# Kernel optimization log

Measured on AMD Instinct MI355X. Metric: run time of the kernel, lower is better.

## Reference

```python
import jax, jax.numpy as jnp
import numpy as np

B, D, L = 2, 1024, 4096   # batch, channels (= num_heads), seq len
FS = 4                    # filter_size
DEPTH = 11                # ceil(log2((L-1)/(FS-1)+1))
LN_EPS = 1e-5


def setup_inputs() -> dict:
    key = jax.random.key(0)
    ks = jax.random.split(key, 7)
    return {
        "x": jax.random.normal(ks[0], (B, D, L), jnp.float32),
        "h0": jax.random.normal(ks[1], (D, 1, FS), jnp.float32) * 0.2,
        "h1": jax.random.normal(ks[2], (D, 1, FS), jnp.float32) * 0.2,
        "w_mix": jax.random.normal(ks[3], (D, D), jnp.float32) / np.sqrt(D),
        "b_mix": jnp.zeros((D,), jnp.float32),
        "ln_gamma": jnp.ones((D,), jnp.float32),
        "ln_beta": jnp.zeros((D,), jnp.float32),
    }


def _dw_conv(a, h, dilation):
    # depthwise (groups = D) dilated conv1d, cross-correlation like torch
    return jax.lax.conv_general_dilated(
        a, h, window_strides=(1,), padding='VALID',
        rhs_dilation=(dilation,),
        dimension_numbers=('NCH', 'OIH', 'NCH'),
        feature_group_count=D)


def reference(x, h0, h1, w_mix, b_mix, ln_gamma, ln_beta):
    # --- multires conv tree ---
    a = x
    dilation = 1
    a_list, b_list = [], []
    for _ in range(DEPTH):
        pad = dilation * (FS - 1)
        ap = jnp.pad(a, ((0, 0), (0, 0), (pad, 0)))  # left causal pad
        b = _dw_conv(ap, h1, dilation)
        a = _dw_conv(ap, h0, dilation)
        a_list.append(a)
        b_list.append(b)
        dilation *= 2
    # --- gated combination across scales (deepest level first) ---
    a_rev = a_list[::-1]
    b_rev = b_list[::-1]
    y = jnp.zeros_like(x)
    gated = None
    for i in range(DEPTH):
        if i + 1 < DEPTH:
            gated = jax.nn.sigmoid(a_rev[i]) * b_rev[i + 1]
        # last iteration reuses the previous gated tensor (matches original)
        y = y + gated
    # --- 1x1 channel mix (Dropout1d is identity in eval) + residual ---
    mixed = jnp.einsum('oc,bcl->bol', w_mix, y) + b_mix[None, :, None]
    z = mixed + x
    # --- LayerNorm over channel dim ---
    mu = jnp.mean(z, axis=1, keepdims=True)
    var = jnp.mean(jnp.square(z - mu), axis=1, keepdims=True)
    out = (z - mu) * jax.lax.rsqrt(var + LN_EPS)
    out = out * ln_gamma[None, :, None] + ln_beta[None, :, None]
    return out
```

## Files before the change

kernel.cpp:

```cpp
#include <hip/hip_runtime.h>
#include <hip/hip_bf16.h>

#define NB 2
#define ND 1024
#define NL 4096
#define NFS 4
#define NDEPTH 11
#define LN_EPS 1e-5f

#define BM 128
#define BN 128
#define BK 32
#define NKI (ND / BK)
#define ASZ (BM * BK)

#define CPAD 3072
#define CBUF (CPAD + NL)

typedef __bf16 bf16x8 __attribute__((ext_vector_type(8)));
typedef float f32x4 __attribute__((ext_vector_type(4)));
typedef _Float16 half8 __attribute__((ext_vector_type(8)));

__device__ __forceinline__ unsigned short f2bf(float f) {
    __hip_bfloat16 h = __float2bfloat16(f);
    unsigned short u;
    __builtin_memcpy(&u, &h, 2);
    return u;
}

__device__ __forceinline__ float bf2f(unsigned short u) {
    unsigned int ui = (unsigned int)u << 16;
    float f;
    __builtin_memcpy(&f, &ui, 4);
    return f;
}

__device__ __forceinline__ unsigned int pack2bf(float lo, float hi) {
    return (unsigned int)f2bf(lo) | ((unsigned int)f2bf(hi) << 16);
}

__device__ __forceinline__ float sigm(float v) {
    return __builtin_amdgcn_rcpf(1.f + __expf(-v));
}

__device__ __forceinline__ void llds16(const void* g, void* l) {
    __builtin_amdgcn_global_load_lds(
        (const __attribute__((address_space(1))) unsigned int*)g,
        (__attribute__((address_space(3))) unsigned int*)l, 16, 0, 0);
}

__global__ __launch_bounds__(256) void wconv_kernel(const float* __restrict__ w,
                                                    unsigned short* __restrict__ wbf) {
    const int idx8 = (blockIdx.x * 256 + threadIdx.x) * 8;
    const float4 v0 = *reinterpret_cast<const float4*>(w + idx8);
    const float4 v1 = *reinterpret_cast<const float4*>(w + idx8 + 4);
    uint4 o;
    o.x = pack2bf(v0.x, v0.y);
    o.y = pack2bf(v0.z, v0.w);
    o.z = pack2bf(v1.x, v1.y);
    o.w = pack2bf(v1.z, v1.w);
    *reinterpret_cast<uint4*>(wbf + idx8) = o;
}

__global__ __launch_bounds__(512, 8) void conv_cascade_kernel(const float* __restrict__ x,
                                                              const float* __restrict__ h0,
                                                              const float* __restrict__ h1,
                                                              unsigned short* __restrict__ ybf) {
    __shared__ _Float16 a_sh[CBUF];
    const int row = blockIdx.x;
    const int d = row & (ND - 1);
    const int t = threadIdx.x;

    if (t < CPAD / 8) *reinterpret_cast<half8*>(&a_sh[t * 8]) = (half8)0;

    const float* xrow = x + (size_t)row * NL;

    _Float16 h0c[NFS], h1c[NFS];
#pragma unroll
    for (int k = 0; k < NFS; ++k) {
        h0c[k] = (_Float16)h0[d * NFS + k];
        h1c[k] = (_Float16)h1[d * NFS + k];
    }

    half8 cur;
    {
        const float4 v0 = *reinterpret_cast<const float4*>(xrow + t * 8);
        const float4 v1 = *reinterpret_cast<const float4*>(xrow + t * 8 + 4);
        cur[0] = (_Float16)v0.x; cur[1] = (_Float16)v0.y;
        cur[2] = (_Float16)v0.z; cur[3] = (_Float16)v0.w;
        cur[4] = (_Float16)v1.x; cur[5] = (_Float16)v1.y;
        cur[6] = (_Float16)v1.z; cur[7] = (_Float16)v1.w;
    }
    const int A = CPAD + t * 8;
    *reinterpret_cast<half8*>(&a_sh[A]) = cur;

    float yacc[8];
    half8 bprev = (half8)0;
#pragma unroll
    for (int j = 0; j < 8; ++j) yacc[j] = 0.f;
    __syncthreads();

    half8 an, bn;

#define CONV_MATH(a1, a2, a3)                                       \
    an = cur * h0c[3] + (a1)*h0c[2] + (a2)*h0c[1] + (a3)*h0c[0];    \
    bn = cur * h1c[3] + (a1)*h1c[2] + (a2)*h1c[1] + (a3)*h1c[0];

#define CONV_FIN(SC)                                                \
    {                                                               \
        *reinterpret_cast<half8*>(&a_sh[A]) = an;                   \
        if ((SC) > 0.f) {                                           \
            _Pragma("unroll") for (int j = 0; j < 8; ++j)           \
                yacc[j] += (SC)*sigm((float)an[j]) * (float)bprev[j]; \
        }                                                           \
        cur = an;                                                   \
        bprev = bn;                                                 \
    }

    {
        const half8 m = *reinterpret_cast<const half8*>(&a_sh[A - 8]);
        const half8 a1 = __builtin_shufflevector(m, cur, 7, 8, 9, 10, 11, 12, 13, 14);
        const half8 a2 = __builtin_shufflevector(m, cur, 6, 7, 8, 9, 10, 11, 12, 13);
        const half8 a3 = __builtin_shufflevector(m, cur, 5, 6, 7, 8, 9, 10, 11, 12);
        CONV_MATH(a1, a2, a3)
        __syncthreads();
        CONV_FIN(0.f)
        __syncthreads();
    }

    {
        const half8 m = *reinterpret_cast<const half8*>(&a_sh[A - 8]);
        const half8 a1 = __builtin_shufflevector(m, cur, 6, 7, 8, 9, 10, 11, 12, 13);
        const half8 a2 = __builtin_shufflevector(m, cur, 4, 5, 6, 7, 8, 9, 10, 11);
        const half8 a3 = __builtin_shufflevector(m, cur, 2, 3, 4, 5, 6, 7, 8, 9);
        CONV_MATH(a1, a2, a3)
        __syncthreads();
        CONV_FIN(2.f)
        __syncthreads();
    }

    {
        const half8 m = *reinterpret_cast<const half8*>(&a_sh[A - 8]);
        const half8 m2 = *reinterpret_cast<const half8*>(&a_sh[A - 16]);
        const half8 a1 = __builtin_shufflevector(m, cur, 4, 5, 6, 7, 8, 9, 10, 11);
        const half8 a2 = m;
        const half8 a3 = __builtin_shufflevector(m2, m, 4, 5, 6, 7, 8, 9, 10, 11);
        CONV_MATH(a1, a2, a3)
        __syncthreads();
        CONV_FIN(1.f)
        __syncthreads();
    }

    int dil = 8;
#pragma unroll 1
    for (int lev = 3; lev <= 9; ++lev) {
        const half8 a1 = *reinterpret_cast<const half8*>(&a_sh[A - dil]);
        const half8 a2 = *reinterpret_cast<const half8*>(&a_sh[A - 2 * dil]);
        const half8 a3 = *reinterpret_cast<const half8*>(&a_sh[A - 3 * dil]);
        CONV_MATH(a1, a2, a3)
        __syncthreads();
        CONV_FIN(1.f)
        dil <<= 1;
        __syncthreads();
    }

    {
        const half8 a1 = *reinterpret_cast<const half8*>(&a_sh[A - 1024]);
        const half8 a2 = *reinterpret_cast<const half8*>(&a_sh[A - 2048]);
        const half8 a3 = *reinterpret_cast<const half8*>(&a_sh[A - 3072]);
        an = cur * h0c[3] + a1 * h0c[2] + a2 * h0c[1] + a3 * h0c[0];
#pragma unroll
        for (int j = 0; j < 8; ++j)
            yacc[j] += sigm((float)an[j]) * (float)bprev[j];
    }
#undef CONV_MATH
#undef CONV_FIN

    uint4 o;
    o.x = pack2bf(yacc[0], yacc[1]);
    o.y = pack2bf(yacc[2], yacc[3]);
    o.z = pack2bf(yacc[4], yacc[5]);
    o.w = pack2bf(yacc[6], yacc[7]);
    *reinterpret_cast<uint4*>(ybf + (size_t)row * NL + t * 8) = o;
}

__global__ __launch_bounds__(256) void transpose_kernel(const unsigned short* __restrict__ ybf,
                                                        unsigned short* __restrict__ yT) {
    __shared__ unsigned short tile[64][66];
    const int l0 = blockIdx.x * 64;
    const int c0 = blockIdx.y * 64;
    const int b = blockIdx.z;
    const int t = threadIdx.x;
    const int li = t & 63, cg = t >> 6;
#pragma unroll
    for (int k = 0; k < 16; ++k) {
        const int ci = cg * 16 + k;
        tile[ci][li] = ybf[(size_t)(b * ND + c0 + ci) * NL + l0 + li];
    }
    __syncthreads();
    const int ci2 = t & 63, lg = t >> 6;
#pragma unroll
    for (int k = 0; k < 16; ++k) {
        const int li2 = lg * 16 + k;
        yT[((size_t)b * NL + l0 + li2) * ND + c0 + ci2] = tile[ci2][li2];
    }
}

__global__ __launch_bounds__(256) void gemm_kernel(const unsigned short* __restrict__ wbf,
                                                   const unsigned short* __restrict__ yT,
                                                   const float* __restrict__ bmix,
                                                   unsigned short* __restrict__ mixed) {
    __shared__ unsigned short As[3][BM][BK];
    __shared__ unsigned short Bs[3][BN][BK];

    const int n0 = blockIdx.x * BN;
    const int m0 = blockIdx.y * BM;
    const int b = blockIdx.z;
    const int t = threadIdx.x;
    const int lane = t & 63, wid = t >> 6;
    const int wr = wid >> 1, wc = wid & 1;
    const int fr = lane & 15;
    const int fk = (lane >> 4) * 8;

    const int srow = wid * 32 + (lane >> 2);
    const int sk = (lane & 3) * 8;
    const unsigned short* Ag = wbf + (size_t)(m0 + srow) * ND + sk;
    const unsigned short* Bg = yT + ((size_t)b * NL + n0 + srow) * ND + sk;
    unsigned short* A0 = &As[0][0][0];
    unsigned short* B0 = &Bs[0][0][0];
    unsigned short* AsW = A0 + wid * 32 * BK;
    unsigned short* BsW = B0 + wid * 32 * BK;

#define STAGE(bo, kt)                           \
    llds16(Ag + (kt), AsW + (bo));              \
    llds16(Ag + (kt) + 16 * ND, AsW + (bo) + 16 * BK); \
    llds16(Bg + (kt), BsW + (bo));              \
    llds16(Bg + (kt) + 16 * ND, BsW + (bo) + 16 * BK);

    f32x4 acc[4][4];
#pragma unroll
    for (int mi = 0; mi < 4; ++mi)
#pragma unroll
        for (int ni = 0; ni < 4; ++ni)
            acc[mi][ni] = (f32x4){0.f, 0.f, 0.f, 0.f};

    STAGE(0, 0)
    STAGE(ASZ, BK)

    int bc = 0;
    int bs = 2;
#pragma unroll 1
    for (int ki = 0; ki < NKI; ++ki) {
        if (ki + 1 < NKI) {
            asm volatile("s_waitcnt vmcnt(4)" ::: "memory");
        } else {
            asm volatile("s_waitcnt vmcnt(0)" ::: "memory");
        }
        __builtin_amdgcn_s_barrier();
        __builtin_amdgcn_sched_barrier(0);

        if (ki + 2 < NKI) {
            const int bo = bs * ASZ;
            const int kt = (ki + 2) * BK;
            STAGE(bo, kt)
        }

        const int bco = bc * ASZ;
        bf16x8 af[4], bv[4];
#pragma unroll
        for (int mi = 0; mi < 4; ++mi)
            af[mi] = *reinterpret_cast<const bf16x8*>(A0 + bco + (wr * 64 + mi * 16 + fr) * BK + fk);
#pragma unroll
        for (int ni = 0; ni < 4; ++ni)
            bv[ni] = *reinterpret_cast<const bf16x8*>(B0 + bco + (wc * 64 + ni * 16 + fr) * BK + fk);
#pragma unroll
        for (int mi = 0; mi < 4; ++mi)
#pragma unroll
            for (int ni = 0; ni < 4; ++ni)
                acc[mi][ni] = __builtin_amdgcn_mfma_f32_16x16x32_bf16(af[mi], bv[ni],
                                                                      acc[mi][ni], 0, 0, 0);
        bc = (bc == 2) ? 0 : bc + 1;
        bs = (bs == 2) ? 0 : bs + 1;
    }
#undef STAGE

    const size_t bbase = (size_t)b * ND * NL;
#pragma unroll
    for (int mi = 0; mi < 4; ++mi) {
#pragma unroll
        for (int r = 0; r < 4; ++r) {
            const int o = m0 + wr * 64 + mi * 16 + (lane >> 4) * 4 + r;
            const float bm = bmix[o];
            const size_t rowbase = bbase + (size_t)o * NL;
#pragma unroll
            for (int ni = 0; ni < 4; ++ni) {
                const int l = n0 + wc * 64 + ni * 16 + fr;
                mixed[rowbase + l] = f2bf(acc[mi][ni][r] + bm);
            }
        }
    }
}

__global__ __launch_bounds__(512) void ln_kernel(const unsigned short* __restrict__ mixed,
                                                 const float* __restrict__ x,
                                                 const float* __restrict__ gamma,
                                                 const float* __restrict__ beta,
                                                 float* __restrict__ out) {
    const int b = blockIdx.y;
    const int l0 = blockIdx.x * 32;
    const int tl = threadIdx.x & 31, tg = threadIdx.x >> 5;
    const size_t base = (size_t)b * ND * NL + l0 + tl;

    float zv[64];
    float s = 0.f, q = 0.f;
#pragma unroll
    for (int j = 0; j < 64; ++j) {
        const size_t idx = base + (size_t)(tg + j * 16) * NL;
        const float v = bf2f(mixed[idx]) + x[idx];
        zv[j] = v;
        s += v;
        q += v * v;
    }

    __shared__ float sred[16][33], qred[16][33];
    __shared__ float mu_s[32], rs_s[32];
    sred[tg][tl] = s;
    qred[tg][tl] = q;
    __syncthreads();
    if (tg == 0) {
        float S = 0.f, Q = 0.f;
#pragma unroll
        for (int g = 0; g < 16; ++g) {
            S += sred[g][tl];
            Q += qred[g][tl];
        }
        const float mu = S * (1.f / ND);
        const float var = Q * (1.f / ND) - mu * mu;
        mu_s[tl] = mu;
        rs_s[tl] = rsqrtf(var + LN_EPS);
    }
    __syncthreads();
    const float mu = mu_s[tl], rs = rs_s[tl];
#pragma unroll
    for (int j = 0; j < 64; ++j) {
        const int c = tg + j * 16;
        out[base + (size_t)c * NL] = (zv[j] - mu) * rs * gamma[c] + beta[c];
    }
}

extern "C" void kernel_launch(void* const* d_in, const int* in_sizes, int n_in,
                              void* d_out, int out_size, void* d_ws, size_t ws_size,
                              hipStream_t stream) {
    (void)in_sizes; (void)n_in; (void)out_size; (void)ws_size;
    const float* x = (const float*)d_in[0];
    const float* h0 = (const float*)d_in[1];
    const float* h1 = (const float*)d_in[2];
    const float* wmix = (const float*)d_in[3];
    const float* bmix = (const float*)d_in[4];
    const float* gamma = (const float*)d_in[5];
    const float* beta = (const float*)d_in[6];
    float* out = (float*)d_out;

    char* ws = (char*)d_ws;
    unsigned short* ybf = (unsigned short*)(ws);
    unsigned short* yT = (unsigned short*)(ws + (size_t)16 * 1024 * 1024);
    unsigned short* wbf = (unsigned short*)(ws + (size_t)32 * 1024 * 1024);
    unsigned short* mixed = (unsigned short*)(ws + (size_t)34 * 1024 * 1024);

    wconv_kernel<<<dim3(ND * ND / (256 * 8)), 256, 0, stream>>>(wmix, wbf);
    conv_cascade_kernel<<<dim3(NB * ND), 512, 0, stream>>>(x, h0, h1, ybf);
    transpose_kernel<<<dim3(NL / 64, ND / 64, NB), 256, 0, stream>>>(ybf, yT);
    gemm_kernel<<<dim3(NL / BN, ND / BM, NB), 256, 0, stream>>>(wbf, yT, bmix, mixed);
    ln_kernel<<<dim3(NL / 32, NB), 512, 0, stream>>>(mixed, x, gamma, beta, out);
}
```

Before: 105.2 us.

## Process both batch rows per conv block and remap GEMM workgroups across XCDs

The conv cascade kernel now handles the same channel for both batch entries in one block. It uses two shared buffers, which halves the number of barriers per row and shares the filter loads. The GEMM launch becomes a 1D grid of 512 blocks with a swizzled mapping so neighbouring blocks, which are spread round-robin over XCDs, share weight and activation tiles in cache. The conv change doubles shared memory per block to about 28 KB and adds register pressure, which may reduce occupancy.

```diff
diff --git a/kernel.cpp b/kernel.cpp
--- a/kernel.cpp
+++ b/kernel.cpp
@@ -66,14 +66,17 @@
                                                               const float* __restrict__ h0,
                                                               const float* __restrict__ h1,
                                                               unsigned short* __restrict__ ybf) {
-    __shared__ _Float16 a_sh[CBUF];
-    const int row = blockIdx.x;
-    const int d = row & (ND - 1);
+    __shared__ _Float16 a_sh[2][CBUF];
+    const int d = blockIdx.x;
     const int t = threadIdx.x;
 
-    if (t < CPAD / 8) *reinterpret_cast<half8*>(&a_sh[t * 8]) = (half8)0;
-
-    const float* xrow = x + (size_t)row * NL;
+    if (t < CPAD / 8) {
+        *reinterpret_cast<half8*>(&a_sh[0][t * 8]) = (half8)0;
+        *reinterpret_cast<half8*>(&a_sh[1][t * 8]) = (half8)0;
+    }
+
+    const float* xrow0 = x + (size_t)d * NL;
+    const float* xrow1 = x + (size_t)(ND + d) * NL;
 
     _Float16 h0c[NFS], h1c[NFS];
 #pragma unroll
@@ -82,106 +85,162 @@
         h1c[k] = (_Float16)h1[d * NFS + k];
     }
 
-    half8 cur;
+    const int A = CPAD + t * 8;
+    half8 cur0, cur1;
     {
-        const float4 v0 = *reinterpret_cast<const float4*>(xrow + t * 8);
-        const float4 v1 = *reinterpret_cast<const float4*>(xrow + t * 8 + 4);
-        cur[0] = (_Float16)v0.x; cur[1] = (_Float16)v0.y;
-        cur[2] = (_Float16)v0.z; cur[3] = (_Float16)v0.w;
-        cur[4] = (_Float16)v1.x; cur[5] = (_Float16)v1.y;
-        cur[6] = (_Float16)v1.z; cur[7] = (_Float16)v1.w;
-    }
-    const int A = CPAD + t * 8;
-    *reinterpret_cast<half8*>(&a_sh[A]) = cur;
-
-    float yacc[8];
-    half8 bprev = (half8)0;
-#pragma unroll
-    for (int j = 0; j < 8; ++j) yacc[j] = 0.f;
+        const float4 v0 = *reinterpret_cast<const float4*>(xrow0 + t * 8);
+        const float4 v1 = *reinterpret_cast<const float4*>(xrow0 + t * 8 + 4);
+        cur0[0] = (_Float16)v0.x; cur0[1] = (_Float16)v0.y;
+        cur0[2] = (_Float16)v0.z; cur0[3] = (_Float16)v0.w;
+        cur0[4] = (_Float16)v1.x; cur0[5] = (_Float16)v1.y;
+        cur0[6] = (_Float16)v1.z; cur0[7] = (_Float16)v1.w;
+        const float4 w0 = *reinterpret_cast<const float4*>(xrow1 + t * 8);
+        const float4 w1 = *reinterpret_cast<const float4*>(xrow1 + t * 8 + 4);
+        cur1[0] = (_Float16)w0.x; cur1[1] = (_Float16)w0.y;
+        cur1[2] = (_Float16)w0.z; cur1[3] = (_Float16)w0.w;
+        cur1[4] = (_Float16)w1.x; cur1[5] = (_Float16)w1.y;
+        cur1[6] = (_Float16)w1.z; cur1[7] = (_Float16)w1.w;
+    }
+    *reinterpret_cast<half8*>(&a_sh[0][A]) = cur0;
+    *reinterpret_cast<half8*>(&a_sh[1][A]) = cur1;
+
+    float yacc0[8], yacc1[8];
+    half8 bprev0 = (half8)0, bprev1 = (half8)0;
+#pragma unroll
+    for (int j = 0; j < 8; ++j) { yacc0[j] = 0.f; yacc1[j] = 0.f; }
     __syncthreads();
 
-    half8 an, bn;
-
-#define CONV_MATH(a1, a2, a3)                                       \
-    an = cur * h0c[3] + (a1)*h0c[2] + (a2)*h0c[1] + (a3)*h0c[0];    \
-    bn = cur * h1c[3] + (a1)*h1c[2] + (a2)*h1c[1] + (a3)*h1c[0];
-
-#define CONV_FIN(SC)                                                \
-    {                                                               \
-        *reinterpret_cast<half8*>(&a_sh[A]) = an;                   \
-        if ((SC) > 0.f) {                                           \
-            _Pragma("unroll") for (int j = 0; j < 8; ++j)           \
+    half8 an0, bn0, an1, bn1;
+
+#define CMATH(cur, a1, a2, a3, an, bn)                                \
+    an = (cur)*h0c[3] + (a1)*h0c[2] + (a2)*h0c[1] + (a3)*h0c[0];      \
+    bn = (cur)*h1c[3] + (a1)*h1c[2] + (a2)*h1c[1] + (a3)*h1c[0];
+
+#define CFIN(r, an, bn, cur, bprev, yacc, SC)                         \
+    {                                                                 \
+        *reinterpret_cast<half8*>(&a_sh[r][A]) = an;                  \
+        if ((SC) > 0.f) {                                             \
+            _Pragma("unroll") for (int j = 0; j < 8; ++j)             \
                 yacc[j] += (SC)*sigm((float)an[j]) * (float)bprev[j]; \
-        }                                                           \
-        cur = an;                                                   \
-        bprev = bn;                                                 \
+        }                                                             \
+        cur = an;                                                     \
+        bprev = bn;                                                   \
     }
 
     {
-        const half8 m = *reinterpret_cast<const half8*>(&a_sh[A - 8]);
-        const half8 a1 = __builtin_shufflevector(m, cur, 7, 8, 9, 10, 11, 12, 13, 14);
-        const half8 a2 = __builtin_shufflevector(m, cur, 6, 7, 8, 9, 10, 11, 12, 13);
-        const half8 a3 = __builtin_shufflevector(m, cur, 5, 6, 7, 8, 9, 10, 11, 12);
-        CONV_MATH(a1, a2, a3)
-        __syncthreads();
-        CONV_FIN(0.f)
+        const half8 m0 = *reinterpret_cast<const half8*>(&a_sh[0][A - 8]);
+        const half8 m1 = *reinterpret_cast<const half8*>(&a_sh[1][A - 8]);
+        {
+            const half8 a1 = __builtin_shufflevector(m0, cur0, 7, 8, 9, 10, 11, 12, 13, 14);
+            const half8 a2 = __builtin_shufflevector(m0, cur0, 6, 7, 8, 9, 10, 11, 12, 13);
+            const half8 a3 = __builtin_shufflevector(m0, cur0, 5, 6, 7, 8, 9, 10, 11, 12);
+            CMATH(cur0, a1, a2, a3, an0, bn0)
+        }
+        {
+            const half8 a1 = __builtin_shufflevector(m1, cur1, 7, 8, 9, 10, 11, 12, 13, 14);
+            const half8 a2 = __builtin_shufflevector(m1, cur1, 6, 7, 8, 9, 10, 11, 12, 13);
+            const half8 a3 = __builtin_shufflevector(m1, cur1, 5, 6, 7, 8, 9, 10, 11, 12);
+            CMATH(cur1, a1, a2, a3, an1, bn1)
+        }
+        __syncthreads();
+        CFIN(0, an0, bn0, cur0, bprev0, yacc0, 0.f)
+        CFIN(1, an1, bn1, cur1, bprev1, yacc1, 0.f)
         __syncthreads();
     }
 
     {
-        const half8 m = *reinterpret_cast<const half8*>(&a_sh[A - 8]);
-        const half8 a1 = __builtin_shufflevector(m, cur, 6, 7, 8, 9, 10, 11, 12, 13);
-        const half8 a2 = __builtin_shufflevector(m, cur, 4, 5, 6, 7, 8, 9, 10, 11);
-        const half8 a3 = __builtin_shufflevector(m, cur, 2, 3, 4, 5, 6, 7, 8, 9);
-        CONV_MATH(a1, a2, a3)
-        __syncthreads();
-        CONV_FIN(2.f)
+        const half8 m0 = *reinterpret_cast<const half8*>(&a_sh[0][A - 8]);
+        const half8 m1 = *reinterpret_cast<const half8*>(&a_sh[1][A - 8]);
+        {
+            const half8 a1 = __builtin_shufflevector(m0, cur0, 6, 7, 8, 9, 10, 11, 12, 13);
+            const half8 a2 = __builtin_shufflevector(m0, cur0, 4, 5, 6, 7, 8, 9, 10, 11);
+            const half8 a3 = __builtin_shufflevector(m0, cur0, 2, 3, 4, 5, 6, 7, 8, 9);
+            CMATH(cur0, a1, a2, a3, an0, bn0)
+        }
+        {
+            const half8 a1 = __builtin_shufflevector(m1, cur1, 6, 7, 8, 9, 10, 11, 12, 13);
+            const half8 a2 = __builtin_shufflevector(m1, cur1, 4, 5, 6, 7, 8, 9, 10, 11);
+            const half8 a3 = __builtin_shufflevector(m1, cur1, 2, 3, 4, 5, 6, 7, 8, 9);
+            CMATH(cur1, a1, a2, a3, an1, bn1)
+        }
+        __syncthreads();
+        CFIN(0, an0, bn0, cur0, bprev0, yacc0, 2.f)
+        CFIN(1, an1, bn1, cur1, bprev1, yacc1, 2.f)
         __syncthreads();
     }
 
     {
-        const half8 m = *reinterpret_cast<const half8*>(&a_sh[A - 8]);
-        const half8 m2 = *reinterpret_cast<const half8*>(&a_sh[A - 16]);
-        const half8 a1 = __builtin_shufflevector(m, cur, 4, 5, 6, 7, 8, 9, 10, 11);
-        const half8 a2 = m;
-        const half8 a3 = __builtin_shufflevector(m2, m, 4, 5, 6, 7, 8, 9, 10, 11);
-        CONV_MATH(a1, a2, a3)
-        __syncthreads();
-        CONV_FIN(1.f)
+        const half8 m0 = *reinterpret_cast<const half8*>(&a_sh[0][A - 8]);
+        const half8 p0 = *reinterpret_cast<const half8*>(&a_sh[0][A - 16]);
+        const half8 m1 = *reinterpret_cast<const half8*>(&a_sh[1][A - 8]);
+        const half8 p1 = *reinterpret_cast<const half8*>(&a_sh[1][A - 16]);
+        {
+            const half8 a1 = __builtin_shufflevector(m0, cur0, 4, 5, 6, 7, 8, 9, 10, 11);
+            const half8 a3 = __builtin_shufflevector(p0, m0, 4, 5, 6, 7, 8, 9, 10, 11);
+            CMATH(cur0, a1, m0, a3, an0, bn0)
+        }
+        {
+            const half8 a1 = __builtin_shufflevector(m1, cur1, 4, 5, 6, 7, 8, 9, 10, 11);
+            const half8 a3 = __builtin_shufflevector(p1, m1, 4, 5, 6, 7, 8, 9, 10, 11);
+            CMATH(cur1, a1, m1, a3, an1, bn1)
+        }
+        __syncthreads();
+        CFIN(0, an0, bn0, cur0, bprev0, yacc0, 1.f)
+        CFIN(1, an1, bn1, cur1, bprev1, yacc1, 1.f)
         __syncthreads();
     }
 
     int dil = 8;
 #pragma unroll 1
     for (int lev = 3; lev <= 9; ++lev) {
-        const half8 a1 = *reinterpret_cast<const half8*>(&a_sh[A - dil]);
-        const half8 a2 = *reinterpret_cast<const half8*>(&a_sh[A - 2 * dil]);
-        const half8 a3 = *reinterpret_cast<const half8*>(&a_sh[A - 3 * dil]);
-        CONV_MATH(a1, a2, a3)
-        __syncthreads();
-        CONV_FIN(1.f)
+        {
+            const half8 a1 = *reinterpret_cast<const half8*>(&a_sh[0][A - dil]);
+            const half8 a2 = *reinterpret_cast<const half8*>(&a_sh[0][A - 2 * dil]);
+            const half8 a3 = *reinterpret_cast<const half8*>(&a_sh[0][A - 3 * dil]);
+            CMATH(cur0, a1, a2, a3, an0, bn0)
+        }
+        {
+            const half8 a1 = *reinterpret_cast<const half8*>(&a_sh[1][A - dil]);
+            const half8 a2 = *reinterpret_cast<const half8*>(&a_sh[1][A - 2 * dil]);
+            const half8 a3 = *reinterpret_cast<const half8*>(&a_sh[1][A - 3 * dil]);
+            CMATH(cur1, a1, a2, a3, an1, bn1)
+        }
+        __syncthreads();
+        CFIN(0, an0, bn0, cur0, bprev0, yacc0, 1.f)
+        CFIN(1, an1, bn1, cur1, bprev1, yacc1, 1.f)
         dil <<= 1;
         __syncthreads();
     }
 
     {
-        const half8 a1 = *reinterpret_cast<const half8*>(&a_sh[A - 1024]);
-        const half8 a2 = *reinterpret_cast<const half8*>(&a_sh[A - 2048]);
-        const half8 a3 = *reinterpret_cast<const half8*>(&a_sh[A - 3072]);
-        an = cur * h0c[3] + a1 * h0c[2] + a2 * h0c[1] + a3 * h0c[0];
-#pragma unroll
-        for (int j = 0; j < 8; ++j)
-            yacc[j] += sigm((float)an[j]) * (float)bprev[j];
-    }
-#undef CONV_MATH
-#undef CONV_FIN
+        const half8 a1 = *reinterpret_cast<const half8*>(&a_sh[0][A - 1024]);
+        const half8 a2 = *reinterpret_cast<const half8*>(&a_sh[0][A - 2048]);
+        const half8 a3 = *reinterpret_cast<const half8*>(&a_sh[0][A - 3072]);
+        an0 = cur0 * h0c[3] + a1 * h0c[2] + a2 * h0c[1] + a3 * h0c[0];
+        const half8 c1 = *reinterpret_cast<const half8*>(&a_sh[1][A - 1024]);
+        const half8 c2 = *reinterpret_cast<const half8*>(&a_sh[1][A - 2048]);
+        const half8 c3 = *reinterpret_cast<const half8*>(&a_sh[1][A - 3072]);
+        an1 = cur1 * h0c[3] + c1 * h0c[2] + c2 * h0c[1] + c3 * h0c[0];
+#pragma unroll
+        for (int j = 0; j < 8; ++j) {
+            yacc0[j] += sigm((float)an0[j]) * (float)bprev0[j];
+            yacc1[j] += sigm((float)an1[j]) * (float)bprev1[j];
+        }
+    }
+#undef CMATH
+#undef CFIN
 
     uint4 o;
-    o.x = pack2bf(yacc[0], yacc[1]);
-    o.y = pack2bf(yacc[2], yacc[3]);
-    o.z = pack2bf(yacc[4], yacc[5]);
-    o.w = pack2bf(yacc[6], yacc[7]);
-    *reinterpret_cast<uint4*>(ybf + (size_t)row * NL + t * 8) = o;
+    o.x = pack2bf(yacc0[0], yacc0[1]);
+    o.y = pack2bf(yacc0[2], yacc0[3]);
+    o.z = pack2bf(yacc0[4], yacc0[5]);
+    o.w = pack2bf(yacc0[6], yacc0[7]);
+    *reinterpret_cast<uint4*>(ybf + (size_t)d * NL + t * 8) = o;
+    o.x = pack2bf(yacc1[0], yacc1[1]);
+    o.y = pack2bf(yacc1[2], yacc1[3]);
+    o.z = pack2bf(yacc1[4], yacc1[5]);
+    o.w = pack2bf(yacc1[6], yacc1[7]);
+    *reinterpret_cast<uint4*>(ybf + (size_t)(ND + d) * NL + t * 8) = o;
 }
 
 __global__ __launch_bounds__(256) void transpose_kernel(const unsigned short* __restrict__ ybf,
@@ -213,9 +272,12 @@
     __shared__ unsigned short As[3][BM][BK];
     __shared__ unsigned short Bs[3][BN][BK];
 
-    const int n0 = blockIdx.x * BN;
-    const int m0 = blockIdx.y * BM;
-    const int b = blockIdx.z;
+    const int orig = blockIdx.x;
+    const int wgid = (orig & 7) * 64 + (orig >> 3);
+    const int b = wgid & 1;
+    const int m0 = ((wgid >> 1) & 7) * BM;
+    const int n0 = (wgid >> 4) * BN;
+
     const int t = threadIdx.x;
     const int lane = t & 63, wid = t >> 6;
     const int wr = wid >> 1, wc = wid & 1;
@@ -368,8 +430,8 @@
     unsigned short* mixed = (unsigned short*)(ws + (size_t)34 * 1024 * 1024);
 
     wconv_kernel<<<dim3(ND * ND / (256 * 8)), 256, 0, stream>>>(wmix, wbf);
-    conv_cascade_kernel<<<dim3(NB * ND), 512, 0, stream>>>(x, h0, h1, ybf);
+    conv_cascade_kernel<<<dim3(ND), 512, 0, stream>>>(x, h0, h1, ybf);
     transpose_kernel<<<dim3(NL / 64, ND / 64, NB), 256, 0, stream>>>(ybf, yT);
-    gemm_kernel<<<dim3(NL / BN, ND / BM, NB), 256, 0, stream>>>(wbf, yT, bmix, mixed);
+    gemm_kernel<<<dim3(512), 256, 0, stream>>>(wbf, yT, bmix, mixed);
     ln_kernel<<<dim3(NL / 32, NB), 512, 0, stream>>>(mixed, x, gamma, beta, out);
 }
```

Measured after the change: 113.5 us. 7.9% more time.
